# Optimization experiments

Hardware: AMD Instinct MI355X
Metric: run time of the kernel (lower is better)

Reference implementation:

```python
import jax, jax.numpy as jnp
import numpy as np

HIDDEN = 256
INPUT = 1
OUTPUT = 1
BATCH = 64
SEQ = 2048


def setup_inputs() -> dict:
    key = jax.random.key(0)
    ks = jax.random.split(key, 8)
    s_ih = 1.0 / np.sqrt(HIDDEN)  # torch nn.LSTM init: U(-1/sqrt(H), 1/sqrt(H))
    x = jax.random.normal(ks[0], (BATCH, SEQ, INPUT), dtype=jnp.float32)
    W_ih = jax.random.uniform(ks[1], (4 * HIDDEN, INPUT), jnp.float32, -s_ih, s_ih)
    W_hh = jax.random.uniform(ks[2], (4 * HIDDEN, HIDDEN), jnp.float32, -s_ih, s_ih)
    b_ih = jax.random.uniform(ks[3], (4 * HIDDEN,), jnp.float32, -s_ih, s_ih)
    b_hh = jax.random.uniform(ks[4], (4 * HIDDEN,), jnp.float32, -s_ih, s_ih)
    W_fc = jax.random.uniform(ks[5], (OUTPUT, HIDDEN), jnp.float32, -s_ih, s_ih)
    b_fc = jax.random.uniform(ks[6], (OUTPUT,), jnp.float32, -s_ih, s_ih)
    return {"x": x, "W_ih": W_ih, "W_hh": W_hh, "b_ih": b_ih,
            "b_hh": b_hh, "W_fc": W_fc, "b_fc": b_fc}


def reference(x, W_ih, W_hh, b_ih, b_hh, W_fc, b_fc):
    B, T, _ = x.shape
    H = W_hh.shape[1]
    # precompute input contribution to all gates: [B,T,4H] (input_dim=1)
    gx = jnp.einsum('bti,gi->btg', x, W_ih) + b_ih + b_hh
    gx_t = jnp.transpose(gx, (1, 0, 2))  # [T,B,4H] for scan over time
    h0 = jnp.zeros((B, H), x.dtype)
    c0 = jnp.zeros((B, H), x.dtype)

    def step(carry, g_t):
        h, c = carry
        gates = g_t + h @ W_hh.T                 # [B,4H]
        i, f, g, o = jnp.split(gates, 4, axis=-1)  # torch gate order i,f,g,o
        i = jax.nn.sigmoid(i)
        f = jax.nn.sigmoid(f)
        g = jnp.tanh(g)
        o = jax.nn.sigmoid(o)
        c = f * c + i * g
        h = o * jnp.tanh(c)
        return (h, c), h

    (h_n, c_n), hs = jax.lax.scan(step, (h0, c0), gx_t)
    out = jnp.transpose(hs, (1, 0, 2))           # [B,T,H]
    y = out @ W_fc.T + b_fc                      # fused linear head [B,T,1]
    return (y, (h_n[None], c_n[None]))           # match torch (num_layers=1, B, H)
```

## Files before the change

kernel.cpp:

```cpp
#include <hip/hip_runtime.h>
#include <hip/hip_fp16.h>

#define SEQT 2048
#define HID  256
#define NB   64

typedef int int32x4 __attribute__((ext_vector_type(4)));
typedef _Float16 h2 __attribute__((ext_vector_type(2)));

#define LOG2E 1.4426950408889634f
static __device__ __forceinline__ float sigf(float x) {
  return __builtin_amdgcn_rcpf(1.f + __builtin_amdgcn_exp2f(-LOG2E * x));
}
static __device__ __forceinline__ float tanhf_fast(float x) {
  float e = __builtin_amdgcn_exp2f(-2.f * LOG2E * fabsf(x));
  float r = (1.f - e) * __builtin_amdgcn_rcpf(1.f + e);
  return copysignf(r, x);
}
static __device__ __forceinline__ float max4(float4 f) {
  return fmaxf(fmaxf(fabsf(f.x), fabsf(f.y)), fmaxf(fabsf(f.z), fabsf(f.w)));
}

__global__ __attribute__((amdgpu_flat_work_group_size(512, 512),
                          amdgpu_waves_per_eu(2, 2)))
void lstm_main(const float* __restrict__ x, const float* __restrict__ Wih,
               const float* __restrict__ Whh, const float* __restrict__ bih,
               const float* __restrict__ bhh, float* __restrict__ out,
               unsigned* __restrict__ hist)
{
  __shared__ __align__(16) unsigned char qring[16 * 256];
  __shared__ __align__(16) unsigned      f16r[16 * 128];
  __shared__ float xs[SEQT];
  __shared__ float rowS[1024];

  const int t    = threadIdx.x;
  const int b    = blockIdx.x;
  const int w    = t >> 6;
  const int lane = t & 63;
  const int ko   = lane >> 4;
  const int lm   = lane & 15;
  const int su   = (lm >> 2) & 1;
  const int ru   = lm & 3;
  const int u    = 32 * w + 16 * su + 4 * ko + ru;

  ((float4*)xs)[t] = ((const float4*)(x + (size_t)b * SEQT))[t];
  if (t < 64) ((unsigned*)qring)[15 * 64 + t] = 0u;

  int32x4 af[8][4];
#pragma unroll
  for (int r = 0; r < 8; ++r) {
    const int q = r >> 1, sh = r & 1;
    const int row = q * 256 + 32 * w + 16 * sh + lm;
    const float* rp = Whh + (size_t)row * HID + 16 * ko;
    float mx = 1e-20f;
#pragma unroll
    for (int kt = 0; kt < 4; ++kt) {
      const float4* p = (const float4*)(rp + 64 * kt);
      mx = fmaxf(mx, fmaxf(fmaxf(max4(p[0]), max4(p[1])),
                           fmaxf(max4(p[2]), max4(p[3]))));
    }
    mx = fmaxf(mx, __shfl_xor(mx, 16, 64));
    mx = fmaxf(mx, __shfl_xor(mx, 32, 64));
    const float winv = 127.f / mx;
    if (ko == 0) rowS[row] = mx * (1.f / (127.f * 127.f));
#pragma unroll
    for (int kt = 0; kt < 4; ++kt) {
      const float4* p = (const float4*)(rp + 64 * kt);
      int32x4 v;
#pragma unroll
      for (int d = 0; d < 4; ++d) {
        float4 f = p[d];
        int q0 = (int)__builtin_rintf(f.x * winv);
        int q1 = (int)__builtin_rintf(f.y * winv);
        int q2 = (int)__builtin_rintf(f.z * winv);
        int q3 = (int)__builtin_rintf(f.w * winv);
        v[d] = (q0 & 255) | ((q1 & 255) << 8) | ((q2 & 255) << 16) | ((q3 & 255) << 24);
      }
      af[r][kt] = v;
    }
  }

  float biasu[4], wihu[4];
#pragma unroll
  for (int q = 0; q < 4; ++q) {
    int row = q * 256 + u;
    biasu[q] = bih[row] + bhh[row];
    wihu[q]  = Wih[row];
  }
  __syncthreads();
  float Su[4];
#pragma unroll
  for (int q = 0; q < 4; ++q) Su[q] = rowS[q * 256 + u];

  unsigned* histb = hist + (size_t)b * SEQT * 128;
  float c = 0.f, h = 0.f;
  const int32x4 z4 = {0, 0, 0, 0};

  for (int s = 0; s < SEQT; ++s) {
    float xv = xs[s];
    const unsigned char* qs = qring + ((s + 15) & 15) * 256;
    int32x4 bf[4];
#pragma unroll
    for (int kt = 0; kt < 4; ++kt)
      bf[kt] = *(const int32x4*)(qs + 64 * kt + 16 * ko);

    int32x4 acc[8];
#pragma unroll
    for (int r = 0; r < 8; ++r)
      acc[r] = __builtin_amdgcn_mfma_i32_16x16x64_i8(af[r][0], bf[0], z4, 0, 0, 0);
#pragma unroll
    for (int kt = 1; kt < 4; ++kt)
#pragma unroll
      for (int r = 0; r < 8; ++r)
        acc[r] = __builtin_amdgcn_mfma_i32_16x16x64_i8(af[r][kt], bf[kt], acc[r], 0, 0, 0);

    float aq[4];
#pragma unroll
    for (int q = 0; q < 4; ++q) {
      int32x4 v0 = acc[2 * q], v1 = acc[2 * q + 1];
      int e0 = su ? v1[0] : v0[0];
      int e1 = su ? v1[1] : v0[1];
      int e2 = su ? v1[2] : v0[2];
      int e3 = su ? v1[3] : v0[3];
      int g01 = (ru & 1) ? e1 : e0;
      int g23 = (ru & 1) ? e3 : e2;
      int gv  = (ru & 2) ? g23 : g01;
      aq[q] = __builtin_fmaf((float)gv, Su[q],
                             __builtin_fmaf(wihu[q], xv, biasu[q]));
    }

    float I = sigf(aq[0]), F = sigf(aq[1]), G = tanhf_fast(aq[2]), O = sigf(aq[3]);
    c = F * c + I * G;
    h = O * tanhf_fast(c);

    if (lm < 8) {
      int qv = (int)__builtin_rintf(h * 127.f);
      ((char*)qring)[(s & 15) * 256 + u]      = (char)qv;
      ((_Float16*)f16r)[(s & 15) * 256 + u]   = (_Float16)h;
    }
    __syncthreads();

    if ((s & 15) == 15) {
      uint4 v = *(const uint4*)(f16r + 4 * t);
      *(uint4*)(histb + (size_t)(s - 15) * 128 + 4 * t) = v;
      __syncthreads();
    }
  }

  if (lm < 8) {
    out[NB * SEQT + b * HID + u]            = h;
    out[NB * SEQT + NB * HID + b * HID + u] = c;
  }
}

__global__ __launch_bounds__(256) void lstm_head(
    const unsigned* __restrict__ hist, const float* __restrict__ Wfc,
    const float* __restrict__ bfc, float* __restrict__ y)
{
  int gw   = (blockIdx.x * 256 + threadIdx.x) >> 6;
  int lane = threadIdx.x & 63;
  uint2 hv = ((const uint2*)(hist + (size_t)gw * 128))[lane];
  float4 w = ((const float4*)Wfc)[lane];
  h2 p0 = __builtin_bit_cast(h2, hv.x);
  h2 p1 = __builtin_bit_cast(h2, hv.y);
  float s = (float)p0.x * w.x + (float)p0.y * w.y +
            (float)p1.x * w.z + (float)p1.y * w.w;
#pragma unroll
  for (int m = 32; m; m >>= 1) s += __shfl_xor(s, m, 64);
  if (lane == 0) y[gw] = s + bfc[0];
}

extern "C" void kernel_launch(void* const* d_in, const int* in_sizes, int n_in,
                              void* d_out, int out_size, void* d_ws, size_t ws_size,
                              hipStream_t stream)
{
  const float* x   = (const float*)d_in[0];
  const float* Wih = (const float*)d_in[1];
  const float* Whh = (const float*)d_in[2];
  const float* bih = (const float*)d_in[3];
  const float* bhh = (const float*)d_in[4];
  const float* Wfc = (const float*)d_in[5];
  const float* bfc = (const float*)d_in[6];
  float* out      = (float*)d_out;
  unsigned* hist  = (unsigned*)d_ws;

  (void)in_sizes; (void)n_in; (void)out_size; (void)ws_size;

  lstm_main<<<dim3(NB), dim3(512), 0, stream>>>(x, Wih, Whh, bih, bhh, out, hist);
  lstm_head<<<dim3((NB * SEQT) / 4), dim3(256), 0, stream>>>(hist, Wfc, bfc, out);
}
```

Baseline: 1.643 ms.

## Process two batch rows per block with interleaved MFMA and activation phases

Each block now carries two independent LSTM sequences, and their steps are interleaved so that one sequence's matrix-multiply phase overlaps the other's activation and quantisation phase. This hides the serial latency chain of MFMA, then activations, then barrier, within a single timestep. The launch is halved to 32 blocks and the shared memory rings are duplicated. The cost is more serial work per block, roughly twice the per-step work on half the CUs, and extra registers for the second accumulator set.

```diff
diff --git a/kernel.cpp b/kernel.cpp
--- a/kernel.cpp
+++ b/kernel.cpp
@@ -28,13 +28,16 @@
                const float* __restrict__ bhh, float* __restrict__ out,
                unsigned* __restrict__ hist)
 {
-  __shared__ __align__(16) unsigned char qring[16 * 256];
-  __shared__ __align__(16) unsigned      f16r[16 * 128];
-  __shared__ float xs[SEQT];
+  __shared__ __align__(16) unsigned char qring0[16 * 256];
+  __shared__ __align__(16) unsigned char qring1[16 * 256];
+  __shared__ __align__(16) unsigned      f16r0[16 * 128];
+  __shared__ __align__(16) unsigned      f16r1[16 * 128];
+  __shared__ float xs0[SEQT], xs1[SEQT];
   __shared__ float rowS[1024];
 
   const int t    = threadIdx.x;
-  const int b    = blockIdx.x;
+  const int bA   = 2 * blockIdx.x;
+  const int bB   = bA + 1;
   const int w    = t >> 6;
   const int lane = t & 63;
   const int ko   = lane >> 4;
@@ -43,8 +46,12 @@
   const int ru   = lm & 3;
   const int u    = 32 * w + 16 * su + 4 * ko + ru;
 
-  ((float4*)xs)[t] = ((const float4*)(x + (size_t)b * SEQT))[t];
-  if (t < 64) ((unsigned*)qring)[15 * 64 + t] = 0u;
+  ((float4*)xs0)[t] = ((const float4*)(x + (size_t)bA * SEQT))[t];
+  ((float4*)xs1)[t] = ((const float4*)(x + (size_t)bB * SEQT))[t];
+  if (t < 64) {
+    ((unsigned*)qring0)[15 * 64 + t] = 0u;
+    ((unsigned*)qring1)[15 * 64 + t] = 0u;
+  }
 
   int32x4 af[8][4];
 #pragma unroll
@@ -92,19 +99,17 @@
 #pragma unroll
   for (int q = 0; q < 4; ++q) Su[q] = rowS[q * 256 + u];
 
-  unsigned* histb = hist + (size_t)b * SEQT * 128;
-  float c = 0.f, h = 0.f;
+  unsigned* histb0 = hist + (size_t)bA * SEQT * 128;
+  unsigned* histb1 = hist + (size_t)bB * SEQT * 128;
+  float cA = 0.f, hA = 0.f, cB = 0.f, hB = 0.f;
   const int32x4 z4 = {0, 0, 0, 0};
-
-  for (int s = 0; s < SEQT; ++s) {
-    float xv = xs[s];
-    const unsigned char* qs = qring + ((s + 15) & 15) * 256;
+  int32x4 accA[8], accB[8];
+
+  auto mfma_phase = [&](const unsigned char* qs, int32x4* acc) {
     int32x4 bf[4];
 #pragma unroll
     for (int kt = 0; kt < 4; ++kt)
       bf[kt] = *(const int32x4*)(qs + 64 * kt + 16 * ko);
-
-    int32x4 acc[8];
 #pragma unroll
     for (int r = 0; r < 8; ++r)
       acc[r] = __builtin_amdgcn_mfma_i32_16x16x64_i8(af[r][0], bf[0], z4, 0, 0, 0);
@@ -113,7 +118,8 @@
 #pragma unroll
       for (int r = 0; r < 8; ++r)
         acc[r] = __builtin_amdgcn_mfma_i32_16x16x64_i8(af[r][kt], bf[kt], acc[r], 0, 0, 0);
-
+  };
+  auto act_phase = [&](int32x4* acc, float xv, float& c, float& h) {
     float aq[4];
 #pragma unroll
     for (int q = 0; q < 4; ++q) {
@@ -128,28 +134,59 @@
       aq[q] = __builtin_fmaf((float)gv, Su[q],
                              __builtin_fmaf(wihu[q], xv, biasu[q]));
     }
-
     float I = sigf(aq[0]), F = sigf(aq[1]), G = tanhf_fast(aq[2]), O = sigf(aq[3]);
     c = F * c + I * G;
     h = O * tanhf_fast(c);
-
+  };
+
+  for (int s = 0; s < SEQT; ++s) {
+    const unsigned char* qs0 = qring0 + ((s + 15) & 15) * 256;
+    if (s) {
+      act_phase(accB, xs1[s - 1], cB, hB);
+      if (lm < 8) {
+        int qv = (int)__builtin_rintf(hB * 127.f);
+        qring1[((s - 1) & 15) * 256 + u]           = (char)qv;
+        ((_Float16*)f16r1)[((s - 1) & 15) * 256 + u] = (_Float16)hB;
+      }
+    }
+    mfma_phase(qs0, accA);
+    __syncthreads();
+
+    if ((s & 15) == 0 && s) {
+      uint4 v = *(const uint4*)(f16r1 + 4 * t);
+      *(uint4*)(histb1 + (size_t)(s - 16) * 128 + 4 * t) = v;
+    }
+
+    const unsigned char* qs1 = qring1 + ((s + 15) & 15) * 256;
+    act_phase(accA, xs0[s], cA, hA);
     if (lm < 8) {
-      int qv = (int)__builtin_rintf(h * 127.f);
-      ((char*)qring)[(s & 15) * 256 + u]      = (char)qv;
-      ((_Float16*)f16r)[(s & 15) * 256 + u]   = (_Float16)h;
-    }
+      int qv = (int)__builtin_rintf(hA * 127.f);
+      qring0[(s & 15) * 256 + u]           = (char)qv;
+      ((_Float16*)f16r0)[(s & 15) * 256 + u] = (_Float16)hA;
+    }
+    mfma_phase(qs1, accB);
     __syncthreads();
 
     if ((s & 15) == 15) {
-      uint4 v = *(const uint4*)(f16r + 4 * t);
-      *(uint4*)(histb + (size_t)(s - 15) * 128 + 4 * t) = v;
-      __syncthreads();
-    }
+      uint4 v = *(const uint4*)(f16r0 + 4 * t);
+      *(uint4*)(histb0 + (size_t)(s - 15) * 128 + 4 * t) = v;
+    }
+  }
+
+  act_phase(accB, xs1[SEQT - 1], cB, hB);
+  if (lm < 8)
+    ((_Float16*)f16r1)[15 * 256 + u] = (_Float16)hB;
+  __syncthreads();
+  {
+    uint4 v = *(const uint4*)(f16r1 + 4 * t);
+    *(uint4*)(histb1 + (size_t)(SEQT - 16) * 128 + 4 * t) = v;
   }
 
   if (lm < 8) {
-    out[NB * SEQT + b * HID + u]            = h;
-    out[NB * SEQT + NB * HID + b * HID + u] = c;
+    out[NB * SEQT + bA * HID + u]            = hA;
+    out[NB * SEQT + bB * HID + u]            = hB;
+    out[NB * SEQT + NB * HID + bA * HID + u] = cA;
+    out[NB * SEQT + NB * HID + bB * HID + u] = cB;
   }
 }
 
@@ -186,6 +223,6 @@
 
   (void)in_sizes; (void)n_in; (void)out_size; (void)ws_size;
 
-  lstm_main<<<dim3(NB), dim3(512), 0, stream>>>(x, Wih, Whh, bih, bhh, out, hist);
+  lstm_main<<<dim3(NB / 2), dim3(512), 0, stream>>>(x, Wih, Whh, bih, bhh, out, hist);
   lstm_head<<<dim3((NB * SEQT) / 4), dim3(256), 0, stream>>>(hist, Wfc, bfc, out);
 }
```

Result: slower. 2.917 ms (+77.5%).

## Split LSTM recurrence across 16 waves with 16 hidden units per wave

Applied to the files above, without the earlier changes.

Doubles the workgroup to 1024 threads so each wave owns 16 hidden units instead of 32. Per step each wave now issues 16 int8 MFMAs instead of 32, and gate extraction is simpler. The cost is a 16-wave barrier every timestep, fewer registers per wave at 4 waves per EU, and only 4 of 16 lanes per group doing useful elementwise work.

```diff
diff --git a/kernel.cpp b/kernel.cpp
--- a/kernel.cpp
+++ b/kernel.cpp
@@ -21,8 +21,8 @@
   return fmaxf(fmaxf(fabsf(f.x), fabsf(f.y)), fmaxf(fabsf(f.z), fabsf(f.w)));
 }
 
-__global__ __attribute__((amdgpu_flat_work_group_size(512, 512),
-                          amdgpu_waves_per_eu(2, 2)))
+__global__ __attribute__((amdgpu_flat_work_group_size(1024, 1024),
+                          amdgpu_waves_per_eu(4, 4)))
 void lstm_main(const float* __restrict__ x, const float* __restrict__ Wih,
                const float* __restrict__ Whh, const float* __restrict__ bih,
                const float* __restrict__ bhh, float* __restrict__ out,
@@ -35,22 +35,20 @@
 
   const int t    = threadIdx.x;
   const int b    = blockIdx.x;
-  const int w    = t >> 6;
+  const int v    = t >> 6;
   const int lane = t & 63;
   const int ko   = lane >> 4;
   const int lm   = lane & 15;
-  const int su   = (lm >> 2) & 1;
   const int ru   = lm & 3;
-  const int u    = 32 * w + 16 * su + 4 * ko + ru;
+  const int u    = 16 * v + 4 * ko + ru;
 
-  ((float4*)xs)[t] = ((const float4*)(x + (size_t)b * SEQT))[t];
+  ((float2*)xs)[t] = ((const float2*)(x + (size_t)b * SEQT))[t];
   if (t < 64) ((unsigned*)qring)[15 * 64 + t] = 0u;
 
-  int32x4 af[8][4];
+  int32x4 af[4][4];
 #pragma unroll
-  for (int r = 0; r < 8; ++r) {
-    const int q = r >> 1, sh = r & 1;
-    const int row = q * 256 + 32 * w + 16 * sh + lm;
+  for (int q = 0; q < 4; ++q) {
+    const int row = q * 256 + 16 * v + lm;
     const float* rp = Whh + (size_t)row * HID + 16 * ko;
     float mx = 1e-20f;
 #pragma unroll
@@ -66,7 +64,7 @@
 #pragma unroll
     for (int kt = 0; kt < 4; ++kt) {
       const float4* p = (const float4*)(rp + 64 * kt);
-      int32x4 v;
+      int32x4 vv;
 #pragma unroll
       for (int d = 0; d < 4; ++d) {
         float4 f = p[d];
@@ -74,9 +72,9 @@
         int q1 = (int)__builtin_rintf(f.y * winv);
         int q2 = (int)__builtin_rintf(f.z * winv);
         int q3 = (int)__builtin_rintf(f.w * winv);
-        v[d] = (q0 & 255) | ((q1 & 255) << 8) | ((q2 & 255) << 16) | ((q3 & 255) << 24);
+        vv[d] = (q0 & 255) | ((q1 & 255) << 8) | ((q2 & 255) << 16) | ((q3 & 255) << 24);
       }
-      af[r][kt] = v;
+      af[q][kt] = vv;
     }
   }
 
@@ -104,27 +102,23 @@
     for (int kt = 0; kt < 4; ++kt)
       bf[kt] = *(const int32x4*)(qs + 64 * kt + 16 * ko);
 
-    int32x4 acc[8];
+    int32x4 acc[4];
 #pragma unroll
-    for (int r = 0; r < 8; ++r)
-      acc[r] = __builtin_amdgcn_mfma_i32_16x16x64_i8(af[r][0], bf[0], z4, 0, 0, 0);
+    for (int q = 0; q < 4; ++q)
+      acc[q] = __builtin_amdgcn_mfma_i32_16x16x64_i8(af[q][0], bf[0], z4, 0, 0, 0);
 #pragma unroll
     for (int kt = 1; kt < 4; ++kt)
 #pragma unroll
-      for (int r = 0; r < 8; ++r)
-        acc[r] = __builtin_amdgcn_mfma_i32_16x16x64_i8(af[r][kt], bf[kt], acc[r], 0, 0, 0);
+      for (int q = 0; q < 4; ++q)
+        acc[q] = __builtin_amdgcn_mfma_i32_16x16x64_i8(af[q][kt], bf[kt], acc[q], 0, 0, 0);
 
     float aq[4];
 #pragma unroll
     for (int q = 0; q < 4; ++q) {
-      int32x4 v0 = acc[2 * q], v1 = acc[2 * q + 1];
-      int e0 = su ? v1[0] : v0[0];
-      int e1 = su ? v1[1] : v0[1];
-      int e2 = su ? v1[2] : v0[2];
-      int e3 = su ? v1[3] : v0[3];
-      int g01 = (ru & 1) ? e1 : e0;
-      int g23 = (ru & 1) ? e3 : e2;
-      int gv  = (ru & 2) ? g23 : g01;
+      int32x4 vv = acc[q];
+      int e01 = (ru & 1) ? vv[1] : vv[0];
+      int e23 = (ru & 1) ? vv[3] : vv[2];
+      int gv  = (ru & 2) ? e23 : e01;
       aq[q] = __builtin_fmaf((float)gv, Su[q],
                              __builtin_fmaf(wihu[q], xv, biasu[q]));
     }
@@ -133,21 +127,23 @@
     c = F * c + I * G;
     h = O * tanhf_fast(c);
 
-    if (lm < 8) {
+    if (lm < 4) {
       int qv = (int)__builtin_rintf(h * 127.f);
-      ((char*)qring)[(s & 15) * 256 + u]      = (char)qv;
-      ((_Float16*)f16r)[(s & 15) * 256 + u]   = (_Float16)h;
+      ((char*)qring)[(s & 15) * 256 + u]    = (char)qv;
+      ((_Float16*)f16r)[(s & 15) * 256 + u] = (_Float16)h;
     }
     __syncthreads();
 
     if ((s & 15) == 15) {
-      uint4 v = *(const uint4*)(f16r + 4 * t);
-      *(uint4*)(histb + (size_t)(s - 15) * 128 + 4 * t) = v;
+      if (t < 512) {
+        uint4 vv = *(const uint4*)(f16r + 4 * t);
+        *(uint4*)(histb + (size_t)(s - 15) * 128 + 4 * t) = vv;
+      }
       __syncthreads();
     }
   }
 
-  if (lm < 8) {
+  if (lm < 4) {
     out[NB * SEQT + b * HID + u]            = h;
     out[NB * SEQT + NB * HID + b * HID + u] = c;
   }
@@ -186,6 +182,6 @@
 
   (void)in_sizes; (void)n_in; (void)out_size; (void)ws_size;
 
-  lstm_main<<<dim3(NB), dim3(512), 0, stream>>>(x, Wih, Whh, bih, bhh, out, hist);
+  lstm_main<<<dim3(NB), dim3(1024), 0, stream>>>(x, Wih, Whh, bih, bhh, out, hist);
   lstm_head<<<dim3((NB * SEQT) / 4), dim3(256), 0, stream>>>(hist, Wfc, bfc, out);
 }
```

Measured after the change: 1.780 ms. +8.3%, slower.
